# Performance work log

Measured on AMD Instinct MI355X. Metric: run time of the kernel, lower is better.

## Reference

```python
import jax, jax.numpy as jnp
import numpy as np

B, S, D_IN, D_OUT = 4, 2048, 1024, 1024

def setup_inputs() -> dict:
    key = jax.random.key(0)
    k_x, k_q, k_k, k_v = jax.random.split(key, 4)
    return {
        "x": jax.random.normal(k_x, (B, S, D_IN), dtype=jnp.float32),
        "W_query": jax.random.uniform(k_q, (D_IN, D_OUT), dtype=jnp.float32),
        "W_key": jax.random.uniform(k_k, (D_IN, D_OUT), dtype=jnp.float32),
        "W_value": jax.random.uniform(k_v, (D_IN, D_OUT), dtype=jnp.float32),
    }

def reference(x, W_query, W_key, W_value):
    seq_len = x.shape[1]
    d_out = W_key.shape[-1]
    # fused QKV projection: x @ concat([Wq, Wk, Wv], -1), then split
    qkv = x @ jnp.concatenate([W_query, W_key, W_value], axis=-1)  # [B,S,3*d_out]
    query, key, value = jnp.split(qkv, 3, axis=2)
    # raw scores [B,S,S]; causal mask applied BEFORE scaling (as in source)
    attn_weights = jnp.einsum("bqd,bkd->bqk", query, key)
    causal = jnp.triu(jnp.ones((seq_len, seq_len), dtype=bool), k=1)
    attn_weights = jnp.where(causal[None, :, :], -jnp.inf, attn_weights)
    scaled = attn_weights / jnp.asarray(d_out, x.dtype) ** 0.5
    attn_scores = jax.nn.softmax(scaled, axis=-1)  # dropout p=0 -> identity
    context_vectors = jnp.einsum("bqk,bkd->bqd", attn_scores, value)
    return (context_vectors, attn_scores)
```

## Files before the change

### kernel.cpp

```cpp
#include <hip/hip_runtime.h>
#include <cstdint>
#include <cstddef>


#define S_LEN 2048
#define D_DIM 1024
#define NBATCH 4
#define MEG (1024 * 1024)

typedef __attribute__((ext_vector_type(4))) float floatx4;
typedef __attribute__((ext_vector_type(8))) __bf16 bf16x8;
typedef __attribute__((ext_vector_type(8))) short short8v;

__device__ __forceinline__ unsigned short f2bf(float f) {
  union { float f; unsigned u; } v; v.f = f;
  unsigned r = v.u + 0x7FFF + ((v.u >> 16) & 1);
  return (unsigned short)(r >> 16);
}
__device__ __forceinline__ float bf2f(unsigned short h) {
  union { unsigned u; float f; } v; v.u = ((unsigned)h) << 16; return v.f;
}

__device__ __forceinline__ void async_copy16(const void* g, void* l) {
  __builtin_amdgcn_global_load_lds(
      (const __attribute__((address_space(1))) void*)g,
      (__attribute__((address_space(3))) void*)l, 16, 0, 0);
}


__device__ __forceinline__ void gemm_bt_core(
    const short* __restrict__ A, const short* __restrict__ B,
    int lda, int ldb, int kIters, int blockM, int blockN,
    short (*As)[32], short (*Bs)[32], floatx4 (&acc)[4][4])
{
  const int tid  = threadIdx.x;
  const int lane = tid & 63;
  const int wave = tid >> 6;
  const int wm = (wave >> 1) * 64;
  const int wn = (wave & 1) * 64;
  const int fm = lane & 15;
  const int fk = (lane >> 4) * 8;
  const int r0 = tid >> 2;
  const int c0 = (tid & 3) * 8;

  floatx4 zero = {0.f, 0.f, 0.f, 0.f};
  #pragma unroll
  for (int i = 0; i < 4; ++i)
    #pragma unroll
    for (int j = 0; j < 4; ++j)
      acc[i][j] = zero;

  const short* a0 = A + (size_t)(blockM + r0) * lda + c0;
  const short* a1 = a0 + (size_t)64 * lda;
  const short* b0 = B + (size_t)(blockN + r0) * ldb + c0;
  const short* b1 = b0 + (size_t)64 * ldb;
  short* as0 = &As[r0][c0];
  short* as1 = &As[r0 + 64][c0];
  short* bs0 = &Bs[r0][c0];
  short* bs1 = &Bs[r0 + 64][c0];

  for (int kt = 0; kt < kIters; ++kt) {
    const int kb = kt * 32;
    async_copy16(a0 + kb, as0);
    async_copy16(a1 + kb, as1);
    async_copy16(b0 + kb, bs0);
    async_copy16(b1 + kb, bs1);
    __syncthreads();
    bf16x8 af[4], bfr[4];
    #pragma unroll
    for (int i = 0; i < 4; ++i)
      af[i] = *(const bf16x8*)(&As[wm + i * 16 + fm][fk]);
    #pragma unroll
    for (int j = 0; j < 4; ++j)
      bfr[j] = *(const bf16x8*)(&Bs[wn + j * 16 + fm][fk]);
    #pragma unroll
    for (int i = 0; i < 4; ++i)
      #pragma unroll
      for (int j = 0; j < 4; ++j)
        acc[i][j] = __builtin_amdgcn_mfma_f32_16x16x32_bf16(af[i], bfr[j], acc[i][j], 0, 0, 0);
    __syncthreads();
  }
}

__device__ __forceinline__ void gemm_bt_split_core(
    const short* __restrict__ Ah, const short* __restrict__ Al,
    const short* __restrict__ Bh, const short* __restrict__ Bl,
    int lda, int ldb, int kIters, int blockM, int blockN,
    short (*AsH)[32], short (*AsL)[32], short (*BsH)[32], short (*BsL)[32],
    floatx4 (&acc)[4][4])
{
  const int tid  = threadIdx.x;
  const int lane = tid & 63;
  const int wave = tid >> 6;
  const int wm = (wave >> 1) * 64;
  const int wn = (wave & 1) * 64;
  const int fm = lane & 15;
  const int fk = (lane >> 4) * 8;
  const int r0 = tid >> 2;
  const int c0 = (tid & 3) * 8;

  floatx4 zero = {0.f, 0.f, 0.f, 0.f};
  #pragma unroll
  for (int i = 0; i < 4; ++i)
    #pragma unroll
    for (int j = 0; j < 4; ++j)
      acc[i][j] = zero;

  const size_t oa0 = (size_t)(blockM + r0) * lda + c0;
  const size_t oa1 = oa0 + (size_t)64 * lda;
  const size_t ob0 = (size_t)(blockN + r0) * ldb + c0;
  const size_t ob1 = ob0 + (size_t)64 * ldb;
  short* lah0 = &AsH[r0][c0]; short* lah1 = &AsH[r0 + 64][c0];
  short* lal0 = &AsL[r0][c0]; short* lal1 = &AsL[r0 + 64][c0];
  short* lbh0 = &BsH[r0][c0]; short* lbh1 = &BsH[r0 + 64][c0];
  short* lbl0 = &BsL[r0][c0]; short* lbl1 = &BsL[r0 + 64][c0];

  for (int kt = 0; kt < kIters; ++kt) {
    const int kb = kt * 32;
    async_copy16(Ah + oa0 + kb, lah0);
    async_copy16(Ah + oa1 + kb, lah1);
    async_copy16(Al + oa0 + kb, lal0);
    async_copy16(Al + oa1 + kb, lal1);
    async_copy16(Bh + ob0 + kb, lbh0);
    async_copy16(Bh + ob1 + kb, lbh1);
    async_copy16(Bl + ob0 + kb, lbl0);
    async_copy16(Bl + ob1 + kb, lbl1);
    __syncthreads();
    bf16x8 ah[4], al[4], bh[4], bl[4];
    #pragma unroll
    for (int i = 0; i < 4; ++i) {
      ah[i] = *(const bf16x8*)(&AsH[wm + i * 16 + fm][fk]);
      al[i] = *(const bf16x8*)(&AsL[wm + i * 16 + fm][fk]);
    }
    #pragma unroll
    for (int j = 0; j < 4; ++j) {
      bh[j] = *(const bf16x8*)(&BsH[wn + j * 16 + fm][fk]);
      bl[j] = *(const bf16x8*)(&BsL[wn + j * 16 + fm][fk]);
    }
    #pragma unroll
    for (int i = 0; i < 4; ++i)
      #pragma unroll
      for (int j = 0; j < 4; ++j) {
        acc[i][j] = __builtin_amdgcn_mfma_f32_16x16x32_bf16(ah[i], bh[j], acc[i][j], 0, 0, 0);
        acc[i][j] = __builtin_amdgcn_mfma_f32_16x16x32_bf16(ah[i], bl[j], acc[i][j], 0, 0, 0);
        acc[i][j] = __builtin_amdgcn_mfma_f32_16x16x32_bf16(al[i], bh[j], acc[i][j], 0, 0, 0);
      }
    __syncthreads();
  }
}


__global__ __launch_bounds__(256) void k_cvt(
    const float4* __restrict__ x,
    const float* __restrict__ wq, const float* __restrict__ wk,
    const float* __restrict__ wv,
    short* __restrict__ xh, short* __restrict__ xl,
    short* __restrict__ wqh, short* __restrict__ wql,
    short* __restrict__ wkh, short* __restrict__ wkl,
    short* __restrict__ wvt, float* __restrict__ muSum)
{
  const int bid = blockIdx.x;
  const int tid = threadIdx.x;
  if (bid < 5120) {
    const float4* src;
    short *dh, *dl;
    size_t idx;
    if (bid < 4096) {
      idx = (size_t)bid * 256 + tid;
      src = x; dh = xh; dl = xl;
    } else if (bid < 4608) {
      idx = (size_t)(bid - 4096) * 256 + tid;
      src = (const float4*)wq; dh = wqh; dl = wql;
    } else {
      idx = (size_t)(bid - 4608) * 256 + tid;
      src = (const float4*)wk; dh = wkh; dl = wkl;
    }
    const float4 u4 = src[idx * 2];
    const float4 w4 = src[idx * 2 + 1];
    float f[8] = {u4.x, u4.y, u4.z, u4.w, w4.x, w4.y, w4.z, w4.w};
    short8v oh, ol;
    #pragma unroll
    for (int e = 0; e < 8; ++e) {
      const unsigned short h = f2bf(f[e]);
      oh[e] = (short)h;
      ol[e] = (short)f2bf(f[e] - bf2f(h));
    }
    *(short8v*)(dh + idx * 8) = oh;
    *(short8v*)(dl + idx * 8) = ol;
  } else {
    if (bid == 5120) {
      float4 z = {0.f, 0.f, 0.f, 0.f};
      ((float4*)muSum)[tid] = z;
    }
    const int rem = bid - 5120;
    const int bx = rem & 31, by = rem >> 5;
    const int tx = tid & 31, ty = tid >> 5;
    __shared__ float tile[32][33];
    const int colIn = bx * 32 + tx;
    #pragma unroll
    for (int i = 0; i < 4; ++i) {
      const int rowIn = by * 32 + ty + i * 8;
      tile[ty + i * 8][tx] = wv[(size_t)rowIn * D_DIM + colIn];
    }
    __syncthreads();
    const int colOut = by * 32 + tx;
    #pragma unroll
    for (int i = 0; i < 4; ++i) {
      const int rowOut = bx * 32 + ty + i * 8;
      wvt[(size_t)rowOut * D_DIM + colOut] = (short)f2bf(tile[tx][ty + i * 8]);
    }
  }
}


__global__ __launch_bounds__(256) void k_gemm_m(
    const short* __restrict__ wqh, const short* __restrict__ wql,
    const short* __restrict__ wkh, const short* __restrict__ wkl,
    short* __restrict__ mth, short* __restrict__ mtl,
    float* __restrict__ muSum)
{
  __shared__ alignas(16) short AsH[128][32];
  __shared__ alignas(16) short AsL[128][32];
  __shared__ alignas(16) short BsH[128][32];
  __shared__ alignas(16) short BsL[128][32];
  floatx4 acc[4][4];
  const int blockM = blockIdx.y * 128;
  const int blockN = blockIdx.x * 128;
  gemm_bt_split_core(wkh, wkl, wqh, wql,
                     D_DIM, D_DIM, D_DIM / 32, blockM, blockN,
                     AsH, AsL, BsH, BsL, acc);

  const int tid = threadIdx.x, lane = tid & 63, wave = tid >> 6;
  const int wm = (wave >> 1) * 64, wn = (wave & 1) * 64;
  const int rb = wm + ((lane >> 4) << 2);
  const int cb = wn + (lane & 15);
  #pragma unroll
  for (int i = 0; i < 4; ++i)
    #pragma unroll
    for (int j = 0; j < 4; ++j) {
      const int n = blockN + cb + j * 16;
      #pragma unroll
      for (int r = 0; r < 4; ++r) {
        const int m = blockM + rb + i * 16 + r;
        const float f = acc[i][j][r];
        const unsigned short h = f2bf(f);
        mth[(size_t)m * D_DIM + n] = (short)h;
        mtl[(size_t)m * D_DIM + n] = (short)f2bf(f - bf2f(h));
      }
    }
  #pragma unroll
  for (int i = 0; i < 4; ++i)
    #pragma unroll
    for (int r = 0; r < 4; ++r) {
      float v = acc[i][0][r] + acc[i][1][r] + acc[i][2][r] + acc[i][3][r];
      v += __shfl_xor(v, 1); v += __shfl_xor(v, 2);
      v += __shfl_xor(v, 4); v += __shfl_xor(v, 8);
      if ((lane & 15) == 0)
        atomicAdd(&muSum[blockM + rb + i * 16 + r], v);
    }
}


__global__ __launch_bounds__(256) void k_rowstats(
    const short* __restrict__ xh, const short* __restrict__ xl,
    const float* __restrict__ muSum, float* __restrict__ sq, float* __restrict__ u)
{
  const int r = blockIdx.x, tid = threadIdx.x;
  const ushort4 h = *(const ushort4*)(xh + (size_t)r * D_DIM + tid * 4);
  const ushort4 l = *(const ushort4*)(xl + (size_t)r * D_DIM + tid * 4);
  const float4 m4 = *(const float4*)(muSum + tid * 4);
  const float x0 = bf2f(h.x) + bf2f(l.x);
  const float x1 = bf2f(h.y) + bf2f(l.y);
  const float x2 = bf2f(h.z) + bf2f(l.z);
  const float x3 = bf2f(h.w) + bf2f(l.w);
  float s = x0 + x1 + x2 + x3;
  float uu = m4.x * x0 + m4.y * x1 + m4.z * x2 + m4.w * x3;
  #pragma unroll
  for (int off = 32; off > 0; off >>= 1) {
    s  += __shfl_xor(s, off);
    uu += __shfl_xor(uu, off);
  }
  __shared__ float ps[4], pu[4];
  if ((tid & 63) == 0) { ps[tid >> 6] = s; pu[tid >> 6] = uu; }
  __syncthreads();
  if (tid == 0) {
    sq[r] = ps[0] + ps[1] + ps[2] + ps[3];
    u[r]  = (pu[0] + pu[1] + pu[2] + pu[3]) * (1.0f / 1024.0f);
  }
}


__global__ __launch_bounds__(256) void k_gemm_nv(
    const short* __restrict__ xh, const short* __restrict__ xl,
    const short* __restrict__ mth, const short* __restrict__ mtl,
    const float* __restrict__ sq, const float* __restrict__ muSum,
    const short* __restrict__ wvt,
    short* __restrict__ nh, short* __restrict__ nl, short* __restrict__ vt)
{
  __shared__ alignas(16) short AsH[128][32];
  __shared__ alignas(16) short AsL[128][32];
  __shared__ alignas(16) short BsH[128][32];
  __shared__ alignas(16) short BsL[128][32];
  floatx4 acc[4][4];

  const int g = blockIdx.x;
  const int id = (g & 7) * 128 + (g >> 3);
  const int idx = id >> 1;
  const int blockM = (idx >> 3) * 128;
  const int blockN = (idx & 7) * 128;

  const int tid = threadIdx.x, lane = tid & 63, wave = tid >> 6;
  const int wm = (wave >> 1) * 64, wn = (wave & 1) * 64;
  const int rb = wm + ((lane >> 4) << 2);
  const int cb = wn + (lane & 15);

  if ((id & 1) == 0) {
    gemm_bt_split_core(xh, xl, mth, mtl, D_DIM, D_DIM, D_DIM / 32,
                       blockM, blockN, AsH, AsL, BsH, BsL, acc);
    #pragma unroll
    for (int i = 0; i < 4; ++i)
      #pragma unroll
      for (int j = 0; j < 4; ++j) {
        const int n = blockN + cb + j * 16;
        const float muv = muSum[n] * (1.0f / 1024.0f);
        #pragma unroll
        for (int r = 0; r < 4; ++r) {
          const int m = blockM + rb + i * 16 + r;
          const float f = acc[i][j][r] - sq[m] * muv;
          const unsigned short h = f2bf(f);
          nh[(size_t)m * D_DIM + n] = (short)h;
          nl[(size_t)m * D_DIM + n] = (short)f2bf(f - bf2f(h));
        }
      }
  } else {
    gemm_bt_core(xh, wvt, D_DIM, D_DIM, D_DIM / 32, blockM, blockN,
                 AsH, BsH, acc);
    #pragma unroll
    for (int i = 0; i < 4; ++i)
      #pragma unroll
      for (int j = 0; j < 4; ++j) {
        const int n = blockN + cb + j * 16;
        const int m0 = blockM + rb + i * 16;
        const int b = m0 >> 11;
        const int s0 = m0 & (S_LEN - 1);
        ushort4 pk;
        pk.x = f2bf(acc[i][j][0]); pk.y = f2bf(acc[i][j][1]);
        pk.z = f2bf(acc[i][j][2]); pk.w = f2bf(acc[i][j][3]);
        *(ushort4*)(vt + ((size_t)b * D_DIM + n) * S_LEN + s0) = pk;
      }
  }
}


__global__ __launch_bounds__(256) void k_gemm_s(
    const short* __restrict__ nh, const short* __restrict__ nl,
    const short* __restrict__ xh, const short* __restrict__ xl,
    const float* __restrict__ sq, const float* __restrict__ u,
    float* __restrict__ attn)
{
  __shared__ alignas(16) short AsH[128][32];
  __shared__ alignas(16) short AsL[128][32];
  __shared__ alignas(16) short BsH[128][32];
  __shared__ alignas(16) short BsL[128][32];
  floatx4 acc[4][4];

  const int g = blockIdx.x;
  const int item = (g & 7) * 68 + (g >> 3);
  const int b = item / 136;
  int t = item - b * 136;
  int band = 0;
  while (t >= 58 - 16 * band) { t -= 58 - 16 * band; ++band; }
  int bi = band * 4;
  for (;;) {
    const int w = bi - band * 4 + 1;
    const int ww = w < 4 ? w : 4;
    if (t < ww) break;
    t -= ww; ++bi;
  }
  const int bj = band * 4 + t;

  const size_t boff = (size_t)b * S_LEN * D_DIM;
  gemm_bt_split_core(nh + boff, nl + boff, xh + boff, xl + boff,
                     D_DIM, D_DIM, D_DIM / 32, bi * 128, bj * 128,
                     AsH, AsL, BsH, BsL, acc);

  float* out = attn + (size_t)b * S_LEN * S_LEN;
  const int tid = threadIdx.x, lane = tid & 63, wave = tid >> 6;
  const int wm = (wave >> 1) * 64, wn = (wave & 1) * 64;
  const int rb = wm + ((lane >> 4) << 2);
  const int cb = wn + (lane & 15);
  const int rowBase = (b << 11) + bi * 128;
  const int colBase = (b << 11) + bj * 128;
  #pragma unroll
  for (int j = 0; j < 4; ++j) {
    const int n = bj * 128 + cb + j * 16;
    const float uv = u[colBase + cb + j * 16];
    #pragma unroll
    for (int i = 0; i < 4; ++i)
      #pragma unroll
      for (int r = 0; r < 4; ++r) {
        const int m = bi * 128 + rb + i * 16 + r;
        const float sv = sq[rowBase + rb + i * 16 + r];
        out[(size_t)m * S_LEN + n] = acc[i][j][r] + sv * uv;
      }
  }
}


__global__ __launch_bounds__(256) void k_softmax(float* __restrict__ attn,
                                                 short* __restrict__ pb) {
  const int b = blockIdx.x >> 11;
  const int q = blockIdx.x & (S_LEN - 1);
  float* row  = attn + ((size_t)b * S_LEN + q) * S_LEN;
  short* prow = pb   + ((size_t)b * S_LEN + q) * S_LEN;
  const int tid = threadIdx.x;
  __shared__ float sMax[4], sSum[4];
  float v[8];
  float mx = -3.0e38f;
  #pragma unroll
  for (int e = 0; e < 8; ++e) {
    const int k = e * 256 + tid;
    v[e] = (k <= q) ? row[k] : -3.0e38f;
    mx = fmaxf(mx, v[e]);
  }
  #pragma unroll
  for (int off = 32; off > 0; off >>= 1) mx = fmaxf(mx, __shfl_xor(mx, off));
  if ((tid & 63) == 0) sMax[tid >> 6] = mx;
  __syncthreads();
  mx = fmaxf(fmaxf(sMax[0], sMax[1]), fmaxf(sMax[2], sMax[3]));

  float s = 0.f;
  #pragma unroll
  for (int e = 0; e < 8; ++e) {
    const int k = e * 256 + tid;
    const float p = (k <= q) ? __expf((v[e] - mx) * 0.03125f) : 0.f;
    v[e] = p;
    s += p;
  }
  #pragma unroll
  for (int off = 32; off > 0; off >>= 1) s += __shfl_xor(s, off);
  if ((tid & 63) == 0) sSum[tid >> 6] = s;
  __syncthreads();
  s = sSum[0] + sSum[1] + sSum[2] + sSum[3];
  const float inv = 1.0f / s;

  #pragma unroll
  for (int e = 0; e < 8; ++e) {
    const int k = e * 256 + tid;
    const float o = v[e] * inv;
    row[k] = o;
    prow[k] = (short)f2bf(o);
  }
}


__global__ __launch_bounds__(256) void k_gemm_ctx(
    const short* __restrict__ pb, const short* __restrict__ vt,
    float* __restrict__ ctx)
{
  __shared__ alignas(16) short As[128][32];
  __shared__ alignas(16) short Bs[64][32];
  floatx4 acc[4][2];
  const int b = blockIdx.z;
  const int by = 15 - blockIdx.y;
  const int blockM = by * 128;
  const int blockN = blockIdx.x * 64;
  const int kIters = by * 4 + 4;
  const short* A = pb + (size_t)b * S_LEN * S_LEN;
  const short* B = vt + (size_t)b * D_DIM * S_LEN;

  const int tid = threadIdx.x, lane = tid & 63, wave = tid >> 6;
  const int wm = (wave >> 1) * 64, wn = (wave & 1) * 32;
  const int fm = lane & 15, fk = (lane >> 4) * 8;
  const int r0 = tid >> 2, c0 = (tid & 3) * 8;

  floatx4 zero = {0.f, 0.f, 0.f, 0.f};
  #pragma unroll
  for (int i = 0; i < 4; ++i)
    #pragma unroll
    for (int j = 0; j < 2; ++j)
      acc[i][j] = zero;

  const short* a0 = A + (size_t)(blockM + r0) * S_LEN + c0;
  const short* a1 = a0 + (size_t)64 * S_LEN;
  const short* b0 = B + (size_t)(blockN + r0) * S_LEN + c0;
  short* as0 = &As[r0][c0];
  short* as1 = &As[r0 + 64][c0];
  short* bs0 = &Bs[r0][c0];

  for (int kt = 0; kt < kIters; ++kt) {
    const int kb = kt * 32;
    async_copy16(a0 + kb, as0);
    async_copy16(a1 + kb, as1);
    async_copy16(b0 + kb, bs0);
    __syncthreads();
    bf16x8 af[4], bfr[2];
    #pragma unroll
    for (int i = 0; i < 4; ++i)
      af[i] = *(const bf16x8*)(&As[wm + i * 16 + fm][fk]);
    #pragma unroll
    for (int j = 0; j < 2; ++j)
      bfr[j] = *(const bf16x8*)(&Bs[wn + j * 16 + fm][fk]);
    #pragma unroll
    for (int i = 0; i < 4; ++i)
      #pragma unroll
      for (int j = 0; j < 2; ++j)
        acc[i][j] = __builtin_amdgcn_mfma_f32_16x16x32_bf16(af[i], bfr[j], acc[i][j], 0, 0, 0);
    __syncthreads();
  }

  float* out = ctx + (size_t)b * S_LEN * D_DIM;
  const int rb = wm + ((lane >> 4) << 2);
  const int cb = wn + (lane & 15);
  #pragma unroll
  for (int i = 0; i < 4; ++i)
    #pragma unroll
    for (int j = 0; j < 2; ++j) {
      const int n = blockN + cb + j * 16;
      #pragma unroll
      for (int r = 0; r < 4; ++r) {
        const int m = blockM + rb + i * 16 + r;
        out[(size_t)m * D_DIM + n] = acc[i][j][r];
      }
    }
}


extern "C" void kernel_launch(void* const* d_in, const int* in_sizes, int n_in,
                              void* d_out, int out_size, void* d_ws, size_t ws_size,
                              hipStream_t stream) {
  const float* x  = (const float*)d_in[0];
  const float* wq = (const float*)d_in[1];
  const float* wk = (const float*)d_in[2];
  const float* wv = (const float*)d_in[3];

  float* out  = (float*)d_out;
  float* ctx  = out;
  float* attn = out + (size_t)NBATCH * S_LEN * D_DIM;

  short* ws  = (short*)d_ws;
  short* xh  = ws;
  short* xl  = xh + (size_t)8 * MEG;
  short* wqh = xl + (size_t)8 * MEG;
  short* wql = wqh + (size_t)1 * MEG;
  short* wkh = wql + (size_t)1 * MEG;
  short* wkl = wkh + (size_t)1 * MEG;
  short* wvt = wkl + (size_t)1 * MEG;
  short* mth = wvt + (size_t)1 * MEG;
  short* mtl = mth + (size_t)1 * MEG;
  short* nh  = mtl + (size_t)1 * MEG;
  short* nl  = nh + (size_t)8 * MEG;
  short* vt  = nl + (size_t)8 * MEG;
  short* pb  = nh;
  float* fb  = (float*)(vt + (size_t)8 * MEG);
  float* muS = fb;
  float* sq  = fb + 1024;
  float* u   = sq + 8192;

  k_cvt<<<6144, 256, 0, stream>>>((const float4*)x, wq, wk, wv,
                                  xh, xl, wqh, wql, wkh, wkl, wvt, muS);
  k_gemm_m<<<dim3(8, 8), 256, 0, stream>>>(wqh, wql, wkh, wkl, mth, mtl, muS);
  k_rowstats<<<8192, 256, 0, stream>>>(xh, xl, muS, sq, u);
  k_gemm_nv<<<1024, 256, 0, stream>>>(xh, xl, mth, mtl, sq, muS, wvt, nh, nl, vt);
  k_gemm_s<<<544, 256, 0, stream>>>(nh, nl, xh, xl, sq, u, attn);
  k_softmax<<<NBATCH * S_LEN, 256, 0, stream>>>(attn, pb);
  k_gemm_ctx<<<dim3(16, 16, 4), 256, 0, stream>>>(pb, vt, ctx);
}
```

Baseline: 428.9 us.

## Split N/V projection kernels, vectorize softmax, widen ctx GEMM tiles

```diff
diff --git a/kernel.cpp b/kernel.cpp
--- a/kernel.cpp
+++ b/kernel.cpp
@@ -290,65 +290,72 @@
 }
 
 
-__global__ __launch_bounds__(256) void k_gemm_nv(
+__global__ __launch_bounds__(256) void k_gemm_n(
     const short* __restrict__ xh, const short* __restrict__ xl,
     const short* __restrict__ mth, const short* __restrict__ mtl,
     const float* __restrict__ sq, const float* __restrict__ muSum,
-    const short* __restrict__ wvt,
-    short* __restrict__ nh, short* __restrict__ nl, short* __restrict__ vt)
+    short* __restrict__ nh, short* __restrict__ nl)
 {
   __shared__ alignas(16) short AsH[128][32];
   __shared__ alignas(16) short AsL[128][32];
   __shared__ alignas(16) short BsH[128][32];
   __shared__ alignas(16) short BsL[128][32];
   floatx4 acc[4][4];
-
-  const int g = blockIdx.x;
-  const int id = (g & 7) * 128 + (g >> 3);
-  const int idx = id >> 1;
-  const int blockM = (idx >> 3) * 128;
-  const int blockN = (idx & 7) * 128;
+  const int blockM = blockIdx.y * 128;
+  const int blockN = blockIdx.x * 128;
+  gemm_bt_split_core(xh, xl, mth, mtl, D_DIM, D_DIM, D_DIM / 32,
+                     blockM, blockN, AsH, AsL, BsH, BsL, acc);
 
   const int tid = threadIdx.x, lane = tid & 63, wave = tid >> 6;
   const int wm = (wave >> 1) * 64, wn = (wave & 1) * 64;
   const int rb = wm + ((lane >> 4) << 2);
   const int cb = wn + (lane & 15);
-
-  if ((id & 1) == 0) {
-    gemm_bt_split_core(xh, xl, mth, mtl, D_DIM, D_DIM, D_DIM / 32,
-                       blockM, blockN, AsH, AsL, BsH, BsL, acc);
-    #pragma unroll
-    for (int i = 0; i < 4; ++i)
+  #pragma unroll
+  for (int i = 0; i < 4; ++i)
+    #pragma unroll
+    for (int j = 0; j < 4; ++j) {
+      const int n = blockN + cb + j * 16;
+      const float muv = muSum[n] * (1.0f / 1024.0f);
       #pragma unroll
-      for (int j = 0; j < 4; ++j) {
-        const int n = blockN + cb + j * 16;
-        const float muv = muSum[n] * (1.0f / 1024.0f);
-        #pragma unroll
-        for (int r = 0; r < 4; ++r) {
-          const int m = blockM + rb + i * 16 + r;
-          const float f = acc[i][j][r] - sq[m] * muv;
-          const unsigned short h = f2bf(f);
-          nh[(size_t)m * D_DIM + n] = (short)h;
-          nl[(size_t)m * D_DIM + n] = (short)f2bf(f - bf2f(h));
-        }
+      for (int r = 0; r < 4; ++r) {
+        const int m = blockM + rb + i * 16 + r;
+        const float f = acc[i][j][r] - sq[m] * muv;
+        const unsigned short h = f2bf(f);
+        nh[(size_t)m * D_DIM + n] = (short)h;
+        nl[(size_t)m * D_DIM + n] = (short)f2bf(f - bf2f(h));
       }
-  } else {
-    gemm_bt_core(xh, wvt, D_DIM, D_DIM, D_DIM / 32, blockM, blockN,
-                 AsH, BsH, acc);
-    #pragma unroll
-    for (int i = 0; i < 4; ++i)
-      #pragma unroll
-      for (int j = 0; j < 4; ++j) {
-        const int n = blockN + cb + j * 16;
-        const int m0 = blockM + rb + i * 16;
-        const int b = m0 >> 11;
-        const int s0 = m0 & (S_LEN - 1);
-        ushort4 pk;
-        pk.x = f2bf(acc[i][j][0]); pk.y = f2bf(acc[i][j][1]);
-        pk.z = f2bf(acc[i][j][2]); pk.w = f2bf(acc[i][j][3]);
-        *(ushort4*)(vt + ((size_t)b * D_DIM + n) * S_LEN + s0) = pk;
-      }
-  }
+    }
+}
+
+
+__global__ __launch_bounds__(256) void k_gemm_v(
+    const short* __restrict__ xh, const short* __restrict__ wvt,
+    short* __restrict__ vt)
+{
+  __shared__ alignas(16) short As[128][32];
+  __shared__ alignas(16) short Bs[128][32];
+  floatx4 acc[4][4];
+  const int blockM = blockIdx.y * 128;
+  const int blockN = blockIdx.x * 128;
+  gemm_bt_core(xh, wvt, D_DIM, D_DIM, D_DIM / 32, blockM, blockN, As, Bs, acc);
+
+  const int tid = threadIdx.x, lane = tid & 63, wave = tid >> 6;
+  const int wm = (wave >> 1) * 64, wn = (wave & 1) * 64;
+  const int rb = wm + ((lane >> 4) << 2);
+  const int cb = wn + (lane & 15);
+  #pragma unroll
+  for (int i = 0; i < 4; ++i)
+    #pragma unroll
+    for (int j = 0; j < 4; ++j) {
+      const int n = blockN + cb + j * 16;
+      const int m0 = blockM + rb + i * 16;
+      const int b = m0 >> 11;
+      const int s0 = m0 & (S_LEN - 1);
+      ushort4 pk;
+      pk.x = f2bf(acc[i][j][0]); pk.y = f2bf(acc[i][j][1]);
+      pk.z = f2bf(acc[i][j][2]); pk.w = f2bf(acc[i][j][3]);
+      *(ushort4*)(vt + ((size_t)b * D_DIM + n) * S_LEN + s0) = pk;
+    }
 }
 
 
@@ -414,13 +421,17 @@
   float* row  = attn + ((size_t)b * S_LEN + q) * S_LEN;
   short* prow = pb   + ((size_t)b * S_LEN + q) * S_LEN;
   const int tid = threadIdx.x;
+  const int k0 = tid * 8;
   __shared__ float sMax[4], sSum[4];
-  float v[8];
+
+  const float4 a0 = *(const float4*)(row + k0);
+  const float4 a1 = *(const float4*)(row + k0 + 4);
+  float v[8] = {a0.x, a0.y, a0.z, a0.w, a1.x, a1.y, a1.z, a1.w};
+
   float mx = -3.0e38f;
   #pragma unroll
   for (int e = 0; e < 8; ++e) {
-    const int k = e * 256 + tid;
-    v[e] = (k <= q) ? row[k] : -3.0e38f;
+    v[e] = (k0 + e <= q) ? v[e] : -3.0e38f;
     mx = fmaxf(mx, v[e]);
   }
   #pragma unroll
@@ -432,8 +443,7 @@
   float s = 0.f;
   #pragma unroll
   for (int e = 0; e < 8; ++e) {
-    const int k = e * 256 + tid;
-    const float p = (k <= q) ? __expf((v[e] - mx) * 0.03125f) : 0.f;
+    const float p = (k0 + e <= q) ? __expf((v[e] - mx) * 0.03125f) : 0.f;
     v[e] = p;
     s += p;
   }
@@ -444,13 +454,18 @@
   s = sSum[0] + sSum[1] + sSum[2] + sSum[3];
   const float inv = 1.0f / s;
 
-  #pragma unroll
-  for (int e = 0; e < 8; ++e) {
-    const int k = e * 256 + tid;
-    const float o = v[e] * inv;
-    row[k] = o;
-    prow[k] = (short)f2bf(o);
-  }
+  float o[8];
+  #pragma unroll
+  for (int e = 0; e < 8; ++e) o[e] = v[e] * inv;
+  float4 w0 = {o[0], o[1], o[2], o[3]};
+  float4 w1 = {o[4], o[5], o[6], o[7]};
+  *(float4*)(row + k0) = w0;
+  *(float4*)(row + k0 + 4) = w1;
+  ushort4 p0, p1;
+  p0.x = f2bf(o[0]); p0.y = f2bf(o[1]); p0.z = f2bf(o[2]); p0.w = f2bf(o[3]);
+  p1.x = f2bf(o[4]); p1.y = f2bf(o[5]); p1.z = f2bf(o[6]); p1.w = f2bf(o[7]);
+  *(ushort4*)(prow + k0) = p0;
+  *(ushort4*)(prow + k0 + 4) = p1;
 }
 
 
@@ -459,63 +474,26 @@
     float* __restrict__ ctx)
 {
   __shared__ alignas(16) short As[128][32];
-  __shared__ alignas(16) short Bs[64][32];
-  floatx4 acc[4][2];
+  __shared__ alignas(16) short Bs[128][32];
+  floatx4 acc[4][4];
   const int b = blockIdx.z;
   const int by = 15 - blockIdx.y;
   const int blockM = by * 128;
-  const int blockN = blockIdx.x * 64;
+  const int blockN = blockIdx.x * 128;
   const int kIters = by * 4 + 4;
   const short* A = pb + (size_t)b * S_LEN * S_LEN;
   const short* B = vt + (size_t)b * D_DIM * S_LEN;
-
+  gemm_bt_core(A, B, S_LEN, S_LEN, kIters, blockM, blockN, As, Bs, acc);
+
+  float* out = ctx + (size_t)b * S_LEN * D_DIM;
   const int tid = threadIdx.x, lane = tid & 63, wave = tid >> 6;
-  const int wm = (wave >> 1) * 64, wn = (wave & 1) * 32;
-  const int fm = lane & 15, fk = (lane >> 4) * 8;
-  const int r0 = tid >> 2, c0 = (tid & 3) * 8;
-
-  floatx4 zero = {0.f, 0.f, 0.f, 0.f};
-  #pragma unroll
-  for (int i = 0; i < 4; ++i)
-    #pragma unroll
-    for (int j = 0; j < 2; ++j)
-      acc[i][j] = zero;
-
-  const short* a0 = A + (size_t)(blockM + r0) * S_LEN + c0;
-  const short* a1 = a0 + (size_t)64 * S_LEN;
-  const short* b0 = B + (size_t)(blockN + r0) * S_LEN + c0;
-  short* as0 = &As[r0][c0];
-  short* as1 = &As[r0 + 64][c0];
-  short* bs0 = &Bs[r0][c0];
-
-  for (int kt = 0; kt < kIters; ++kt) {
-    const int kb = kt * 32;
-    async_copy16(a0 + kb, as0);
-    async_copy16(a1 + kb, as1);
-    async_copy16(b0 + kb, bs0);
-    __syncthreads();
-    bf16x8 af[4], bfr[2];
-    #pragma unroll
-    for (int i = 0; i < 4; ++i)
-      af[i] = *(const bf16x8*)(&As[wm + i * 16 + fm][fk]);
-    #pragma unroll
-    for (int j = 0; j < 2; ++j)
-      bfr[j] = *(const bf16x8*)(&Bs[wn + j * 16 + fm][fk]);
-    #pragma unroll
-    for (int i = 0; i < 4; ++i)
-      #pragma unroll
-      for (int j = 0; j < 2; ++j)
-        acc[i][j] = __builtin_amdgcn_mfma_f32_16x16x32_bf16(af[i], bfr[j], acc[i][j], 0, 0, 0);
-    __syncthreads();
-  }
-
-  float* out = ctx + (size_t)b * S_LEN * D_DIM;
+  const int wm = (wave >> 1) * 64, wn = (wave & 1) * 64;
   const int rb = wm + ((lane >> 4) << 2);
   const int cb = wn + (lane & 15);
   #pragma unroll
   for (int i = 0; i < 4; ++i)
     #pragma unroll
-    for (int j = 0; j < 2; ++j) {
+    for (int j = 0; j < 4; ++j) {
       const int n = blockN + cb + j * 16;
       #pragma unroll
       for (int r = 0; r < 4; ++r) {
@@ -561,8 +539,9 @@
                                   xh, xl, wqh, wql, wkh, wkl, wvt, muS);
   k_gemm_m<<<dim3(8, 8), 256, 0, stream>>>(wqh, wql, wkh, wkl, mth, mtl, muS);
   k_rowstats<<<8192, 256, 0, stream>>>(xh, xl, muS, sq, u);
-  k_gemm_nv<<<1024, 256, 0, stream>>>(xh, xl, mth, mtl, sq, muS, wvt, nh, nl, vt);
+  k_gemm_n<<<dim3(8, 64), 256, 0, stream>>>(xh, xl, mth, mtl, sq, muS, nh, nl);
+  k_gemm_v<<<dim3(8, 64), 256, 0, stream>>>(xh, wvt, vt);
   k_gemm_s<<<544, 256, 0, stream>>>(nh, nl, xh, xl, sq, u, attn);
   k_softmax<<<NBATCH * S_LEN, 256, 0, stream>>>(attn, pb);
-  k_gemm_ctx<<<dim3(16, 16, 4), 256, 0, stream>>>(pb, vt, ctx);
-}
+  k_gemm_ctx<<<dim3(8, 16, 4), 256, 0, stream>>>(pb, vt, ctx);
+}
```

After: 431.8 us. Within noise of the previous version (+0.7%).
